# Kernel optimization log

Hardware: AMD Instinct MI355X
Metric: run time of the kernel (lower is better)

Reference implementation:

```python
import jax, jax.numpy as jnp
import numpy as np

N_ITERS = 7
N_NODE_FEAT = 10   # GRU hidden size
N_NODE_IN = 9
N_EDGE_FEAT = 11
N_OUT = 2
MSG = 96


def setup_inputs() -> dict:
    key = jax.random.key(0)
    ks = jax.random.split(key, 20)
    N, E = 20000, 320000

    def lin(k, fan_in, fan_out):
        b = 1.0 / np.sqrt(fan_in)
        kw, kb = jax.random.split(k)
        W = jax.random.uniform(kw, (fan_out, fan_in), jnp.float32, -b, b)
        bias = jax.random.uniform(kb, (fan_out,), jnp.float32, -b, b)
        return W, bias

    W1, b1 = lin(ks[0], 2 * N_NODE_FEAT + N_EDGE_FEAT, MSG)
    W2, b2 = lin(ks[1], MSG, MSG)
    W3, b3 = lin(ks[2], MSG, MSG)
    W4, b4 = lin(ks[3], MSG, N_EDGE_FEAT)
    gru_in = N_EDGE_FEAT + N_NODE_IN
    gru_wih, gru_bih = lin(ks[4], gru_in, 3 * N_NODE_FEAT)
    gru_whh, gru_bhh = lin(ks[5], N_NODE_FEAT, 3 * N_NODE_FEAT)
    fin_w, fin_b = lin(ks[6], N_NODE_FEAT, N_OUT)

    return {
        'node_inputs': jax.random.normal(ks[7], (N, N_NODE_IN), jnp.float32),
        'edge_attr': jax.random.normal(ks[8], (E, N_EDGE_FEAT), jnp.float32),
        'W1': W1, 'b1': b1, 'W2': W2, 'b2': b2, 'W3': W3, 'b3': b3,
        'W4': W4, 'b4': b4,
        'gru_wih': gru_wih, 'gru_whh': gru_whh,
        'gru_bih': gru_bih, 'gru_bhh': gru_bhh,
        'fin_w': fin_w, 'fin_b': fin_b,
        'src_ids': jax.random.randint(ks[9], (E,), 0, N, jnp.int32),
        'dst_ids': jax.random.randint(ks[10], (E,), 0, N, jnp.int32),
    }


def reference(node_inputs, edge_attr, W1, b1, W2, b2, W3, b3, W4, b4,
              gru_wih, gru_whh, gru_bih, gru_bhh, fin_w, fin_b,
              src_ids, dst_ids):
    N = node_inputs.shape[0]
    H = gru_whh.shape[1]  # n_node_features

    def step(h, _):
        # edge MLP on gathered endpoint states  [E, 2H+F] -> [E, F]
        m = jnp.concatenate([h[src_ids], h[dst_ids], edge_attr], axis=1)
        m = jax.nn.relu(m @ W1.T + b1)
        m = jax.nn.relu(m @ W2.T + b2)
        m = jax.nn.relu(m @ W3.T + b3)
        msg = m @ W4.T + b4
        # scatter-add messages to destination nodes  [N, F]
        agg = jax.ops.segment_sum(msg, dst_ids, num_segments=N)
        # GRU cell (PyTorch gate order: r, z, n)
        x = jnp.concatenate([agg, node_inputs], axis=1)
        gi = x @ gru_wih.T + gru_bih
        gh = h @ gru_whh.T + gru_bhh
        i_r, i_z, i_n = jnp.split(gi, 3, axis=1)
        h_r, h_z, h_n = jnp.split(gh, 3, axis=1)
        r = jax.nn.sigmoid(i_r + h_r)
        z = jax.nn.sigmoid(i_z + h_z)
        n = jnp.tanh(i_n + r * h_n)
        h_new = (1.0 - z) * n + z * h
        logits = h_new @ fin_w.T + fin_b  # [N, 2]
        return h_new, logits

    h0 = jnp.zeros((N, H), node_inputs.dtype)
    _, outs = jax.lax.scan(step, h0, None, length=N_ITERS)
    return outs  # [T, N, 2]
```

## Files before the change

### kernel.cpp

```cpp
#include <hip/hip_runtime.h>
#include <math.h>
#include <stdint.h>

typedef _Float16 f16;
typedef f16 f16x8 __attribute__((ext_vector_type(8)));
typedef f16 f16x4 __attribute__((ext_vector_type(4)));
typedef float f32x4 __attribute__((ext_vector_type(4)));

#define N_ITERS 7
#define HF 10
#define NIN 9
#define EF 11
#define GIN (EF + NIN)

#define S1 40
#define S2 104
#define G  4
#define MSTR 12
#define RSTR 40

#define LPN 8

union FragU { f16x8 v; uint32_t u[4]; uint2 p2[2]; uint4 q4; };

__device__ __forceinline__ int sigmap(int k) {
    return 32 * (k >> 5) + 16 * ((k >> 2) & 1) + 4 * ((k >> 3) & 3) + (k & 3);
}

__global__ __launch_bounds__(256) void convert_weights(
    const float* __restrict__ W1, const float* __restrict__ W2,
    const float* __restrict__ W3, const float* __restrict__ W4,
    f16* __restrict__ wf)
{
    f16* wf1 = wf;
    f16* wf2 = wf1 + 96 * S1;
    f16* wf3 = wf2 + 96 * S2;
    f16* wf4 = wf3 + 96 * S2;
    const int tid = blockIdx.x * 256 + threadIdx.x;
    const int nt = gridDim.x * 256;
    for (int i = tid; i < 96 * S1; i += nt) {
        int m = i / S1, k = i % S1;
        wf1[i] = (k < 31) ? (f16)W1[m * 31 + k] : (f16)0.f;
    }
    for (int i = tid; i < 96 * S2; i += nt) {
        int m = i / S2, k = i % S2;
        wf2[i] = (k < 96) ? (f16)W2[m * 96 + sigmap(k)] : (f16)0.f;
        wf3[i] = (k < 96) ? (f16)W3[m * 96 + sigmap(k)] : (f16)0.f;
    }
    for (int i = tid; i < 16 * S2; i += nt) {
        int m = i / S2, k = i % S2;
        wf4[i] = (m < 11 && k < 96) ? (f16)W4[m * 96 + sigmap(k)] : (f16)0.f;
    }
}

__global__ __launch_bounds__(256) void count_edges(
    const int* __restrict__ dst, int* __restrict__ cnt, int E)
{
    int e = blockIdx.x * 256 + threadIdx.x;
    if (e < E) atomicAdd(&cnt[dst[e]], 1);
}

__global__ __launch_bounds__(1024) void scan_counts(
    const int* __restrict__ cnt, int* __restrict__ row_ptr,
    int* __restrict__ nxt, int N, int E)
{
    __shared__ int sums[1024];
    const int tid = threadIdx.x;
    const int C = (N + 1023) >> 10;
    const int base = tid * C;
    int local = 0;
    for (int i = 0; i < C; ++i) {
        int idx = base + i;
        if (idx < N) local += cnt[idx];
    }
    sums[tid] = local;
    __syncthreads();
    for (int off = 1; off < 1024; off <<= 1) {
        int v = (tid >= off) ? sums[tid - off] : 0;
        __syncthreads();
        sums[tid] += v;
        __syncthreads();
    }
    int run = sums[tid] - local;
    for (int i = 0; i < C; ++i) {
        int idx = base + i;
        if (idx < N) {
            row_ptr[idx] = run;
            nxt[idx] = run;
            run += cnt[idx];
        }
    }
    if (tid == 0) row_ptr[N] = E;
}

__global__ __launch_bounds__(256) void scatter_edges(
    const int* __restrict__ dst, int* __restrict__ nxt,
    int* __restrict__ perm, int E)
{
    int e = blockIdx.x * 256 + threadIdx.x;
    if (e < E) {
        int pos = atomicAdd(&nxt[dst[e]], 1);
        perm[pos] = e;
    }
}

__global__ __launch_bounds__(256) void pack_edges(
    const int* __restrict__ perm, const int* __restrict__ src,
    const int* __restrict__ dst, const float* __restrict__ ea,
    int* __restrict__ srcs, int* __restrict__ dsts,
    f16* __restrict__ eaA, f16* __restrict__ eaB, int E)
{
    int i = blockIdx.x * 256 + threadIdx.x;
    if (i >= E) return;
    int e = perm[i];
    srcs[i] = src[e];
    dsts[i] = dst[e];
    const float* r = ea + (size_t)e * EF;
    f16x4 a;
#pragma unroll
    for (int j = 0; j < 4; ++j) a[j] = (f16)r[j];
    *(f16x4*)(eaA + (size_t)i * 4) = a;
    f16x8 b;
#pragma unroll
    for (int j = 0; j < 7; ++j) b[j] = (f16)r[4 + j];
    b[7] = (f16)0.f;
    *(f16x8*)(eaB + (size_t)i * 8) = b;
}

__device__ __forceinline__ uint32_t pack_relu2(float x, float y) {
    union { f16 h[2]; uint32_t u; } r;
    r.h[0] = (f16)fmaxf(x, 0.0f);
    r.h[1] = (f16)fmaxf(y, 0.0f);
    return r.u;
}

__global__ __launch_bounds__(256, 2) void edge_mlp_mfma(
    const f16* __restrict__ h16, const f16* __restrict__ wf,
    const float* __restrict__ b1, const float* __restrict__ b2,
    const float* __restrict__ b3, const float* __restrict__ b4,
    const int* __restrict__ srcs, const int* __restrict__ dsts,
    const f16* __restrict__ eaA, const f16* __restrict__ eaB,
    float* __restrict__ msg, int E)
{
    const f16* wf1 = wf;
    const f16* wf2 = wf1 + 96 * S1;
    const f16* wf3 = wf2 + 96 * S2;
    const f16* wf4 = wf3 + 96 * S2;

    __shared__ f16 rec[256][RSTR];

    const int wave = threadIdx.x >> 6;
    const int lane = threadIdx.x & 63;
    const int n = lane & 15;
    const int q = lane >> 4;

    const int i0 = blockIdx.x * 256 + wave * (G * 16);

    {
        const int tid = threadIdx.x;
        const int i = blockIdx.x * 256 + tid;
        const int ii = (i < E) ? i : 0;
        const int s = srcs[ii];
        const int d = dsts[ii];
        const uint4* h16q = (const uint4*)h16;
        const uint32_t* h16u = (const uint32_t*)h16;
        uint4 hs0 = h16q[(size_t)s * 2];
        uint32_t hs1 = h16u[(size_t)s * 8 + 4];
        uint4 hd0 = h16q[(size_t)d * 2];
        uint32_t hd1 = h16u[(size_t)d * 8 + 4];
        uint2 ea0 = ((const uint2*)eaA)[ii];
        uint4 ea1 = ((const uint4*)eaB)[ii];
        uint4 w1 = { hs1, hd0.x, hd0.y, hd0.z };
        uint4 w2 = { hd0.w, hd1, ea0.x, ea0.y };
        uint4* rp = (uint4*)&rec[tid][0];
        rp[0] = hs0;
        rp[1] = w1;
        rp[2] = w2;
        rp[3] = ea1;
    }
    __syncthreads();

    FragU bfr[G][3];

    {
        f16x8 a[6];
#pragma unroll
        for (int t = 0; t < 6; ++t)
            a[t] = *(const f16x8*)(wf1 + (t * 16 + n) * S1 + 8 * q);
        f32x4 bias[6];
#pragma unroll
        for (int t = 0; t < 6; ++t)
            bias[t] = *(const f32x4*)(b1 + t * 16 + 4 * q);
        FragU bf[G];
#pragma unroll
        for (int g = 0; g < G; ++g)
            bf[g].v = *(const f16x8*)&rec[wave * 64 + g * 16 + n][q * 8];
#pragma unroll
        for (int g = 0; g < G; ++g) {
#pragma unroll
            for (int t = 0; t < 6; ++t) {
                f32x4 c = __builtin_amdgcn_mfma_f32_16x16x32_f16(a[t], bf[g].v, bias[t], 0, 0, 0);
                bfr[g][t >> 1].u[2 * (t & 1) + 0] = pack_relu2(c[0], c[1]);
                bfr[g][t >> 1].u[2 * (t & 1) + 1] = pack_relu2(c[2], c[3]);
            }
        }
    }

    const f16* wmid[2] = { wf2, wf3 };
    const float* bmid[2] = { b2, b3 };
#pragma unroll 1
    for (int L = 0; L < 2; ++L) {
        const f16* w = wmid[L];
        const float* bb = bmid[L];
        f16x8 a[18];
#pragma unroll
        for (int t = 0; t < 6; ++t)
#pragma unroll
            for (int kb = 0; kb < 3; ++kb)
                a[t * 3 + kb] = *(const f16x8*)(w + (t * 16 + n) * S2 + kb * 32 + 8 * q);
        f32x4 bias[6];
#pragma unroll
        for (int t = 0; t < 6; ++t)
            bias[t] = *(const f32x4*)(bb + t * 16 + 4 * q);
#pragma unroll
        for (int g = 0; g < G; ++g) {
            FragU nf[3];
#pragma unroll
            for (int t = 0; t < 6; ++t) {
                f32x4 c = bias[t];
#pragma unroll
                for (int kb = 0; kb < 3; ++kb)
                    c = __builtin_amdgcn_mfma_f32_16x16x32_f16(a[t * 3 + kb], bfr[g][kb].v, c, 0, 0, 0);
                nf[t >> 1].u[2 * (t & 1) + 0] = pack_relu2(c[0], c[1]);
                nf[t >> 1].u[2 * (t & 1) + 1] = pack_relu2(c[2], c[3]);
            }
#pragma unroll
            for (int kb = 0; kb < 3; ++kb)
                bfr[g][kb] = nf[kb];
        }
    }

    {
        f16x8 a[3];
#pragma unroll
        for (int kb = 0; kb < 3; ++kb)
            a[kb] = *(const f16x8*)(wf4 + n * S2 + kb * 32 + 8 * q);
        float bias[4];
#pragma unroll
        for (int r = 0; r < 4; ++r) {
            const int m = 4 * q + r;
            bias[r] = (m < 11) ? b4[m] : 0.0f;
        }
#pragma unroll
        for (int g = 0; g < G; ++g) {
            f32x4 c = { bias[0], bias[1], bias[2], bias[3] };
#pragma unroll
            for (int kb = 0; kb < 3; ++kb)
                c = __builtin_amdgcn_mfma_f32_16x16x32_f16(a[kb], bfr[g][kb].v, c, 0, 0, 0);
            const int ig = i0 + g * 16 + n;
            if (q < 3 && ig < E)
                *(f32x4*)(msg + (size_t)ig * MSTR + 4 * q) = c;
        }
    }
}

__global__ __launch_bounds__(256) void gru_node_kernel(
    const float* __restrict__ node_inputs,
    float* __restrict__ h, f16* __restrict__ h16,
    const int* __restrict__ row_ptr, const float* __restrict__ msg,
    const float* __restrict__ wih, const float* __restrict__ whh,
    const float* __restrict__ bih, const float* __restrict__ bhh,
    const float* __restrict__ fw, const float* __restrict__ fb,
    float* __restrict__ out_t, int N)
{
    const int T = blockIdx.x * blockDim.x + threadIdx.x;
    const int n = T / LPN;
    const int sub = T & (LPN - 1);
    if (n >= N) return;

    float x[GIN];
#pragma unroll
    for (int k = 0; k < EF; ++k) x[k] = 0.0f;
    const int r0 = row_ptr[n], r1 = row_ptr[n + 1];
    for (int r = r0 + sub; r < r1; r += LPN) {
        const f32x4* mp = (const f32x4*)(msg + (size_t)r * MSTR);
        f32x4 a = mp[0], b = mp[1], c = mp[2];
        x[0] += a[0]; x[1] += a[1]; x[2] += a[2]; x[3] += a[3];
        x[4] += b[0]; x[5] += b[1]; x[6] += b[2]; x[7] += b[3];
        x[8] += c[0]; x[9] += c[1]; x[10] += c[2];
    }
#pragma unroll
    for (int off = 1; off < LPN; off <<= 1) {
#pragma unroll
        for (int k = 0; k < EF; ++k)
            x[k] += __shfl_xor(x[k], off);
    }
#pragma unroll
    for (int k = 0; k < NIN; ++k) x[EF + k] = node_inputs[(size_t)n * NIN + k];

    float hv[HF];
#pragma unroll
    for (int k = 0; k < HF; ++k) hv[k] = h[(size_t)n * HF + k];

    float hn[HF];
#pragma unroll
    for (int k = 0; k < HF; ++k) {
        float gir = bih[k];
        float giz = bih[HF + k];
        float gin = bih[2 * HF + k];
        float ghr = bhh[k];
        float ghz = bhh[HF + k];
        float ghn = bhh[2 * HF + k];
#pragma unroll
        for (int kk = 0; kk < GIN; ++kk) {
            gir = fmaf(x[kk], wih[(size_t)k * GIN + kk], gir);
            giz = fmaf(x[kk], wih[(size_t)(HF + k) * GIN + kk], giz);
            gin = fmaf(x[kk], wih[(size_t)(2 * HF + k) * GIN + kk], gin);
        }
#pragma unroll
        for (int kk = 0; kk < HF; ++kk) {
            ghr = fmaf(hv[kk], whh[(size_t)k * HF + kk], ghr);
            ghz = fmaf(hv[kk], whh[(size_t)(HF + k) * HF + kk], ghz);
            ghn = fmaf(hv[kk], whh[(size_t)(2 * HF + k) * HF + kk], ghn);
        }
        const float r2 = 1.0f / (1.0f + __expf(-(gir + ghr)));
        const float z  = 1.0f / (1.0f + __expf(-(giz + ghz)));
        const float nn = tanhf(gin + r2 * ghn);
        hn[k] = (1.0f - z) * nn + z * hv[k];
    }

    if (sub == 0) {
#pragma unroll
        for (int k = 0; k < HF; ++k) h[(size_t)n * HF + k] = hn[k];
        union { f16 hh[8]; uint4 q; } p4;
#pragma unroll
        for (int k = 0; k < 8; ++k) p4.hh[k] = (f16)hn[k];
        *(uint4*)(h16 + (size_t)n * 16) = p4.q;
        union { f16 hh[2]; uint32_t u; } p1;
        p1.hh[0] = (f16)hn[8]; p1.hh[1] = (f16)hn[9];
        *(uint32_t*)(h16 + (size_t)n * 16 + 8) = p1.u;

        float l0 = fb[0], l1 = fb[1];
#pragma unroll
        for (int k = 0; k < HF; ++k) {
            l0 = fmaf(hn[k], fw[k], l0);
            l1 = fmaf(hn[k], fw[HF + k], l1);
        }
        float2 lo = { l0, l1 };
        *(float2*)(out_t + (size_t)n * 2) = lo;
    }
}

extern "C" void kernel_launch(void* const* d_in, const int* in_sizes, int n_in,
                              void* d_out, int out_size, void* d_ws, size_t ws_size,
                              hipStream_t stream) {
    const float* node_inputs = (const float*)d_in[0];
    const float* edge_attr   = (const float*)d_in[1];
    const float* W1 = (const float*)d_in[2];
    const float* b1 = (const float*)d_in[3];
    const float* W2 = (const float*)d_in[4];
    const float* b2 = (const float*)d_in[5];
    const float* W3 = (const float*)d_in[6];
    const float* b3 = (const float*)d_in[7];
    const float* W4 = (const float*)d_in[8];
    const float* b4 = (const float*)d_in[9];
    const float* gru_wih = (const float*)d_in[10];
    const float* gru_whh = (const float*)d_in[11];
    const float* gru_bih = (const float*)d_in[12];
    const float* gru_bhh = (const float*)d_in[13];
    const float* fin_w   = (const float*)d_in[14];
    const float* fin_b   = (const float*)d_in[15];
    const int* src_ids = (const int*)d_in[16];
    const int* dst_ids = (const int*)d_in[17];

    const int N = in_sizes[0] / NIN;
    const int E = in_sizes[1] / EF;

    char* base = (char*)d_ws;
    size_t off = 0;
    auto alloc = [&](size_t bytes) -> char* {
        char* p = base + off;
        off += (bytes + 255) & ~(size_t)255;
        return p;
    };
    float* msg    = (float*)alloc((size_t)E * MSTR * 4);
    f16*   eaB    = (f16*)  alloc((size_t)E * 8 * 2);
    f16*   eaA    = (f16*)  alloc((size_t)E * 4 * 2);
    f16*   h16    = (f16*)  alloc((size_t)N * 16 * 2);
    float* hbuf   = (float*)alloc((size_t)N * HF * 4);
    f16*   wf     = (f16*)  alloc(52000 * 2);
    int*   row_ptr= (int*)  alloc((size_t)(N + 1) * 4);
    int*   cnt    = (int*)  alloc((size_t)N * 4);
    int*   nxt    = (int*)  alloc((size_t)N * 4);
    int*   perm   = (int*)  alloc((size_t)E * 4);
    int*   srcs   = (int*)  alloc((size_t)E * 4);
    int*   dsts   = (int*)  alloc((size_t)E * 4);

    const int eb = (E + 255) / 256;
    const int nb = (N * LPN + 255) / 256;

    hipMemsetAsync(h16, 0, (size_t)N * 16 * 2, stream);
    hipMemsetAsync(hbuf, 0, (size_t)N * HF * 4, stream);
    hipMemsetAsync(cnt, 0, (size_t)N * 4, stream);
    convert_weights<<<60, 256, 0, stream>>>(W1, W2, W3, W4, wf);
    count_edges<<<eb, 256, 0, stream>>>(dst_ids, cnt, E);
    scan_counts<<<1, 1024, 0, stream>>>(cnt, row_ptr, nxt, N, E);
    scatter_edges<<<eb, 256, 0, stream>>>(dst_ids, nxt, perm, E);
    pack_edges<<<eb, 256, 0, stream>>>(perm, src_ids, dst_ids, edge_attr,
                                       srcs, dsts, eaA, eaB, E);

    float* out = (float*)d_out;
    for (int t = 0; t < N_ITERS; ++t) {
        edge_mlp_mfma<<<eb, 256, 0, stream>>>(
            h16, wf, b1, b2, b3, b4, srcs, dsts, eaA, eaB, msg, E);
        gru_node_kernel<<<nb, 256, 0, stream>>>(
            node_inputs, hbuf, h16, row_ptr, msg,
            gru_wih, gru_whh, gru_bih, gru_bhh,
            fin_w, fin_b, out + (size_t)t * N * 2, N);
    }
}
```

Measured before the change: 504.9 us.

## Fuse edge scatter and pack, merge memsets, raise edge MLP occupancy

Merges the scatter_edges and pack_edges kernels into one scatter_pack kernel, so each edge writes its packed data straight to its CSR slot and the perm array is no longer needed. Reorders workspace allocations so the three zeroing memsets become one contiguous memset. Raises the launch bounds minimum blocks per CU for edge_mlp_mfma from 2 to 4, which may force register limits and cause spills. Writes become scattered instead of coalesced, and edge order within a node stays nondeterministic as before.

```diff
diff --git a/kernel.cpp b/kernel.cpp
--- a/kernel.cpp
+++ b/kernel.cpp
@@ -93,38 +93,28 @@
     if (tid == 0) row_ptr[N] = E;
 }
 
-__global__ __launch_bounds__(256) void scatter_edges(
-    const int* __restrict__ dst, int* __restrict__ nxt,
-    int* __restrict__ perm, int E)
-{
-    int e = blockIdx.x * 256 + threadIdx.x;
-    if (e < E) {
-        int pos = atomicAdd(&nxt[dst[e]], 1);
-        perm[pos] = e;
-    }
-}
-
-__global__ __launch_bounds__(256) void pack_edges(
-    const int* __restrict__ perm, const int* __restrict__ src,
-    const int* __restrict__ dst, const float* __restrict__ ea,
+__global__ __launch_bounds__(256) void scatter_pack(
+    const int* __restrict__ src, const int* __restrict__ dst,
+    const float* __restrict__ ea, int* __restrict__ nxt,
     int* __restrict__ srcs, int* __restrict__ dsts,
     f16* __restrict__ eaA, f16* __restrict__ eaB, int E)
 {
-    int i = blockIdx.x * 256 + threadIdx.x;
-    if (i >= E) return;
-    int e = perm[i];
-    srcs[i] = src[e];
-    dsts[i] = dst[e];
+    int e = blockIdx.x * 256 + threadIdx.x;
+    if (e >= E) return;
+    const int d = dst[e];
+    const int pos = atomicAdd(&nxt[d], 1);
+    srcs[pos] = src[e];
+    dsts[pos] = d;
     const float* r = ea + (size_t)e * EF;
     f16x4 a;
 #pragma unroll
     for (int j = 0; j < 4; ++j) a[j] = (f16)r[j];
-    *(f16x4*)(eaA + (size_t)i * 4) = a;
+    *(f16x4*)(eaA + (size_t)pos * 4) = a;
     f16x8 b;
 #pragma unroll
     for (int j = 0; j < 7; ++j) b[j] = (f16)r[4 + j];
     b[7] = (f16)0.f;
-    *(f16x8*)(eaB + (size_t)i * 8) = b;
+    *(f16x8*)(eaB + (size_t)pos * 8) = b;
 }
 
 __device__ __forceinline__ uint32_t pack_relu2(float x, float y) {
@@ -134,7 +124,7 @@
     return r.u;
 }
 
-__global__ __launch_bounds__(256, 2) void edge_mlp_mfma(
+__global__ __launch_bounds__(256, 4) void edge_mlp_mfma(
     const f16* __restrict__ h16, const f16* __restrict__ wf,
     const float* __restrict__ b1, const float* __restrict__ b2,
     const float* __restrict__ b3, const float* __restrict__ b4,
@@ -388,26 +378,23 @@
     f16*   eaA    = (f16*)  alloc((size_t)E * 4 * 2);
     f16*   h16    = (f16*)  alloc((size_t)N * 16 * 2);
     float* hbuf   = (float*)alloc((size_t)N * HF * 4);
+    int*   cnt    = (int*)  alloc((size_t)N * 4);
     f16*   wf     = (f16*)  alloc(52000 * 2);
     int*   row_ptr= (int*)  alloc((size_t)(N + 1) * 4);
-    int*   cnt    = (int*)  alloc((size_t)N * 4);
     int*   nxt    = (int*)  alloc((size_t)N * 4);
-    int*   perm   = (int*)  alloc((size_t)E * 4);
     int*   srcs   = (int*)  alloc((size_t)E * 4);
     int*   dsts   = (int*)  alloc((size_t)E * 4);
 
     const int eb = (E + 255) / 256;
     const int nb = (N * LPN + 255) / 256;
 
-    hipMemsetAsync(h16, 0, (size_t)N * 16 * 2, stream);
-    hipMemsetAsync(hbuf, 0, (size_t)N * HF * 4, stream);
-    hipMemsetAsync(cnt, 0, (size_t)N * 4, stream);
+    const size_t zspan = (size_t)((char*)cnt + (size_t)N * 4 - (char*)h16);
+    hipMemsetAsync(h16, 0, zspan, stream);
     convert_weights<<<60, 256, 0, stream>>>(W1, W2, W3, W4, wf);
     count_edges<<<eb, 256, 0, stream>>>(dst_ids, cnt, E);
     scan_counts<<<1, 1024, 0, stream>>>(cnt, row_ptr, nxt, N, E);
-    scatter_edges<<<eb, 256, 0, stream>>>(dst_ids, nxt, perm, E);
-    pack_edges<<<eb, 256, 0, stream>>>(perm, src_ids, dst_ids, edge_attr,
-                                       srcs, dsts, eaA, eaB, E);
+    scatter_pack<<<eb, 256, 0, stream>>>(src_ids, dst_ids, edge_attr, nxt,
+                                         srcs, dsts, eaA, eaB, E);
 
     float* out = (float*)d_out;
     for (int t = 0; t < N_ITERS; ++t) {
```

Result: slower. 771.9 us (+52.9%).
